# Optimization experiments

Hardware: AMD Instinct MI355X
Metric: run time of the kernel (lower is better)

Reference implementation:

```python
import jax, jax.numpy as jnp
import numpy as np

B, S, D = 2, 2048, 2048
H, KV, HD = 8, 1, 256          # num_heads, num_kv_heads, head_dim
ROPE_BASE = 10000.0
NEG_INF = -1e9


def _rope_cos_sin(position_ids, head_dim, base):
    # position_ids: [B, S] -> cos/sin: [B, S, head_dim]
    inv_freq = 1.0 / (base ** (jnp.arange(0, head_dim, 2, dtype=jnp.float32) / head_dim))
    freqs = position_ids.astype(jnp.float32)[..., None] * inv_freq  # [B,S,HD/2]
    emb = jnp.concatenate([freqs, freqs], axis=-1)                  # [B,S,HD]
    return jnp.cos(emb), jnp.sin(emb)


def _rotate_half(x):
    h = x.shape[-1] // 2
    return jnp.concatenate([-x[..., h:], x[..., :h]], axis=-1)


def _apply_rope(x, cos, sin):
    # x: [B,h,S,HD]; cos/sin: [B,S,HD]
    c = cos[:, None, :, :]
    s = sin[:, None, :, :]
    return x * c + _rotate_half(x) * s


def setup_inputs() -> dict:
    key = jax.random.key(0)
    ks = jax.random.split(key, 6)
    hidden_state = jax.random.normal(ks[0], (B, S, D), dtype=jnp.float32)
    # additive causal mask: 0 on/below diagonal, -inf above
    causal = jnp.tril(jnp.ones((S, S), dtype=bool))
    attention_mask = jnp.where(causal, 0.0, NEG_INF).astype(jnp.float32)[None, None]  # [B?1,1,S,S]
    attention_mask = jnp.broadcast_to(attention_mask, (B, 1, S, S))
    position_ids = jnp.broadcast_to(jnp.arange(S, dtype=jnp.int64)[None, :], (B, S))
    scale = 0.02
    Wq = jax.random.normal(ks[1], (D, H * HD), dtype=jnp.float32) * scale
    Wk = jax.random.normal(ks[2], (D, KV * HD), dtype=jnp.float32) * scale
    Wv = jax.random.normal(ks[3], (D, KV * HD), dtype=jnp.float32) * scale
    Wo = jax.random.normal(ks[4], (H * HD, D), dtype=jnp.float32) * scale
    return {"hidden_state": hidden_state, "attention_mask": attention_mask,
            "position_ids": position_ids, "Wq": Wq, "Wk": Wk, "Wv": Wv, "Wo": Wo}


def reference(hidden_state, attention_mask, position_ids, Wq, Wk, Wv, Wo):
    bsz, q_len, _ = hidden_state.shape
    n_rep = H // KV
    # projections
    q = (hidden_state @ Wq).reshape(bsz, q_len, H, HD).transpose(0, 2, 1, 3)   # [B,H,S,HD]
    k = (hidden_state @ Wk).reshape(bsz, q_len, KV, HD).transpose(0, 2, 1, 3)  # [B,KV,S,HD]
    v = (hidden_state @ Wv).reshape(bsz, q_len, KV, HD).transpose(0, 2, 1, 3)
    # RoPE
    cos, sin = _rope_cos_sin(position_ids, HD, ROPE_BASE)
    q = _apply_rope(q, cos, sin)
    k = _apply_rope(k, cos, sin)
    # GQA: repeat kv heads
    k = jnp.repeat(k, n_rep, axis=1)  # [B,H,S,HD]
    v = jnp.repeat(v, n_rep, axis=1)
    # eager attention with full score matrix (faithful to source)
    scores = jnp.einsum('bhqd,bhkd->bhqk', q, k) / jnp.sqrt(jnp.float32(HD))
    scores = scores + attention_mask
    attn = jax.nn.softmax(scores.astype(jnp.float32), axis=-1).astype(q.dtype)
    out = jnp.einsum('bhqk,bhkd->bhqd', attn, v)            # [B,H,S,HD]
    out = out.transpose(0, 2, 1, 3).reshape(bsz, q_len, H * HD)
    return out @ Wo
```

## Files before the change

### kernel.cpp

```cpp
#include <hip/hip_runtime.h>
#include <cstdint>
#include <cstddef>

#define B_   2
#define S_   2048
#define D_   2048
#define H_   8
#define HD_  256
#define M_   (B_ * S_)
#define NQ_  (H_ * HD_)
#define NKV_ 256

typedef unsigned short u16;
typedef __attribute__((ext_vector_type(8))) short short8v;
typedef __attribute__((ext_vector_type(4))) float f32x4;

__device__ __forceinline__ u16 f2bf_rn(float x) {
    unsigned int u = __float_as_uint(x);
    unsigned int r = u + 0x7FFFu + ((u >> 16) & 1u);
    return (u16)(r >> 16);
}
__device__ __forceinline__ float bf2f(u16 h) {
    return __uint_as_float(((unsigned int)h) << 16);
}

__device__ __forceinline__ void gll16(const u16* g, u16* l) {
    __builtin_amdgcn_global_load_lds(
        (const __attribute__((address_space(1))) void*)(g),
        (__attribute__((address_space(3))) void*)(l), 16, 0, 0);
}

__global__ __launch_bounds__(256) void split_kernel(const float* __restrict__ in,
                                                    u16* __restrict__ hi,
                                                    u16* __restrict__ lo)
{
    const size_t i = ((size_t)blockIdx.x * 256 + threadIdx.x) * 8;
    float4 v0 = *(const float4*)(in + i);
    float4 v1 = *(const float4*)(in + i + 4);
    float xs[8] = {v0.x, v0.y, v0.z, v0.w, v1.x, v1.y, v1.z, v1.w};
    unsigned int hv[4], lv[4];
#pragma unroll
    for (int k = 0; k < 4; ++k) {
        u16 h0 = f2bf_rn(xs[2 * k]);
        u16 h1 = f2bf_rn(xs[2 * k + 1]);
        u16 l0 = f2bf_rn(xs[2 * k] - bf2f(h0));
        u16 l1 = f2bf_rn(xs[2 * k + 1] - bf2f(h1));
        hv[k] = (unsigned int)h0 | ((unsigned int)h1 << 16);
        lv[k] = (unsigned int)l0 | ((unsigned int)l1 << 16);
    }
    *(uint4*)(hi + i) = make_uint4(hv[0], hv[1], hv[2], hv[3]);
    *(uint4*)(lo + i) = make_uint4(lv[0], lv[1], lv[2], lv[3]);
}

__global__ __launch_bounds__(256) void tsplit_kernel(const float* __restrict__ W,
                                                     u16* __restrict__ Th,
                                                     u16* __restrict__ Tl,
                                                     int K, int N)
{
    __shared__ float t[64][65];
    const int kt = blockIdx.x, nt = blockIdx.y;
    const int c4 = (threadIdx.x & 15) * 4;
    const int r  = threadIdx.x >> 4;

#pragma unroll
    for (int s = 0; s < 4; ++s) {
        const int kk = r + s * 16;
        float4 v = *(const float4*)(W + (size_t)(kt * 64 + kk) * N + nt * 64 + c4);
        t[kk][c4 + 0] = v.x;
        t[kk][c4 + 1] = v.y;
        t[kk][c4 + 2] = v.z;
        t[kk][c4 + 3] = v.w;
    }
    __syncthreads();
#pragma unroll
    for (int s = 0; s < 4; ++s) {
        const int nn = r + s * 16;
        unsigned int hv[2], lv[2];
#pragma unroll
        for (int p = 0; p < 2; ++p) {
            u16 h0, h1, l0, l1;
            float x0 = t[c4 + 2 * p][nn];
            float x1 = t[c4 + 2 * p + 1][nn];
            h0 = f2bf_rn(x0); l0 = f2bf_rn(x0 - bf2f(h0));
            h1 = f2bf_rn(x1); l1 = f2bf_rn(x1 - bf2f(h1));
            hv[p] = (unsigned int)h0 | ((unsigned int)h1 << 16);
            lv[p] = (unsigned int)l0 | ((unsigned int)l1 << 16);
        }
        u16* ph = Th + (size_t)(nt * 64 + nn) * K + kt * 64 + c4;
        u16* pl = Tl + (size_t)(nt * 64 + nn) * K + kt * 64 + c4;
        *(uint2*)ph = make_uint2(hv[0], hv[1]);
        *(uint2*)pl = make_uint2(lv[0], lv[1]);
    }
}

__device__ __forceinline__ void mfma_gemm_tile(
    const u16* __restrict__ Ah, const u16* __restrict__ Al,
    const u16* __restrict__ Bh, const u16* __restrict__ Bl,
    float* __restrict__ C, const int Kd, const int ldc,
    const int bm0, const int bn0)
{
    __shared__ u16 ldsAh[128 * 32];
    __shared__ u16 ldsAl[128 * 32];
    __shared__ u16 ldsBh[128 * 32];
    __shared__ u16 ldsBl[128 * 32];

    const int tid  = threadIdx.x;
    const int lane = tid & 63;
    const int w    = tid >> 6;
    const int wr   = w >> 1, wc = w & 1;

    const int srow = w * 32 + (lane >> 2);
    const int schk = (lane & 3) * 8;
    const u16* gAh = Ah + (size_t)(bm0 + srow) * Kd + schk;
    const u16* gAl = Al + (size_t)(bm0 + srow) * Kd + schk;
    const u16* gBh = Bh + (size_t)(bn0 + srow) * Kd + schk;
    const u16* gBl = Bl + (size_t)(bn0 + srow) * Kd + schk;

    f32x4 acc[4][4];
#pragma unroll
    for (int i = 0; i < 4; ++i)
#pragma unroll
        for (int j = 0; j < 4; ++j) acc[i][j] = (f32x4){0.f, 0.f, 0.f, 0.f};

    const int fr = lane & 15;
    const int kb = (lane >> 4) * 8;

    for (int k0 = 0; k0 < Kd; k0 += 32) {
        if (k0) __syncthreads();
#pragma unroll
        for (int c = 0; c < 2; ++c) {
            const size_t go = (size_t)(c * 16) * Kd + k0;
            const int lb = (w * 32 + c * 16) * 32;
            gll16(gAh + go, &ldsAh[lb]);
            gll16(gAl + go, &ldsAl[lb]);
            gll16(gBh + go, &ldsBh[lb]);
            gll16(gBl + go, &ldsBl[lb]);
        }
        __syncthreads();

        short8v a_h[4], a_l[4], b_h[4], b_l[4];
#pragma unroll
        for (int f = 0; f < 4; ++f) {
            const int ra = (wr * 64 + f * 16 + fr) * 32 + kb;
            const int rb = (wc * 64 + f * 16 + fr) * 32 + kb;
            a_h[f] = *(const short8v*)&ldsAh[ra];
            a_l[f] = *(const short8v*)&ldsAl[ra];
            b_h[f] = *(const short8v*)&ldsBh[rb];
            b_l[f] = *(const short8v*)&ldsBl[rb];
        }
#pragma unroll
        for (int i = 0; i < 4; ++i)
#pragma unroll
            for (int j = 0; j < 4; ++j) {
                acc[i][j] = __builtin_amdgcn_mfma_f32_16x16x32_bf16(a_h[i], b_h[j], acc[i][j], 0, 0, 0);
                acc[i][j] = __builtin_amdgcn_mfma_f32_16x16x32_bf16(a_h[i], b_l[j], acc[i][j], 0, 0, 0);
                acc[i][j] = __builtin_amdgcn_mfma_f32_16x16x32_bf16(a_l[i], b_h[j], acc[i][j], 0, 0, 0);
            }
    }

    const int cr = (lane >> 4) * 4;
    const int cc = lane & 15;
#pragma unroll
    for (int i = 0; i < 4; ++i)
#pragma unroll
        for (int j = 0; j < 4; ++j) {
#pragma unroll
            for (int r = 0; r < 4; ++r) {
                C[(size_t)(bm0 + wr * 64 + i * 16 + cr + r) * ldc
                  + (bn0 + wc * 64 + j * 16 + cc)] = acc[i][j][r];
            }
        }
}

__global__ __launch_bounds__(256, 2) void qkv_mfma_kernel(
    const u16* __restrict__ Xh, const u16* __restrict__ Xl,
    const u16* __restrict__ WqTh, const u16* __restrict__ WqTl,
    const u16* __restrict__ WkTh, const u16* __restrict__ WkTl,
    const u16* __restrict__ WvTh, const u16* __restrict__ WvTl,
    float* __restrict__ Qo, float* __restrict__ Ko, float* __restrict__ Vo)
{
    const int bn = blockIdx.x;
    const u16 *Bh, *Bl; float* C; int ldc, col0;
    if (bn < 16)      { Bh = WqTh; Bl = WqTl; C = Qo; ldc = NQ_;  col0 = bn * 128; }
    else if (bn < 18) { Bh = WkTh; Bl = WkTl; C = Ko; ldc = NKV_; col0 = (bn - 16) * 128; }
    else              { Bh = WvTh; Bl = WvTl; C = Vo; ldc = NKV_; col0 = (bn - 18) * 128; }
    mfma_gemm_tile(Xh, Xl, Bh, Bl, C, D_, ldc, blockIdx.y * 128, col0);
}

__global__ __launch_bounds__(256, 2) void out_mfma_kernel(
    const u16* __restrict__ Ch, const u16* __restrict__ Cl,
    const u16* __restrict__ WoTh, const u16* __restrict__ WoTl,
    float* __restrict__ Out)
{
    mfma_gemm_tile(Ch, Cl, WoTh, WoTl, Out, NQ_, D_, blockIdx.y * 128, blockIdx.x * 128);
}

__global__ __launch_bounds__(128) void rope_split_q_kernel(
    const float* __restrict__ Qw, u16* __restrict__ Qh, u16* __restrict__ Ql)
{
    const int row = blockIdx.x;
    const int d = threadIdx.x;
    const int s = row & (S_ - 1);

    const float expo = (float)(2 * d) / (float)HD_;
    const float inv_freq = 1.0f / powf(10000.0f, expo);
    float sn, c;
    sincosf((float)s * inv_freq, &sn, &c);

    const float* qr = Qw + (size_t)row * NQ_;
    u16* qhr = Qh + (size_t)row * NQ_;
    u16* qlr = Ql + (size_t)row * NQ_;
#pragma unroll
    for (int h = 0; h < H_; ++h) {
        float x0 = qr[h * HD_ + d];
        float x1 = qr[h * HD_ + d + 128];
        float y0 = x0 * c - x1 * sn;
        float y1 = x1 * c + x0 * sn;
        u16 h0 = f2bf_rn(y0), h1 = f2bf_rn(y1);
        qhr[h * HD_ + d]       = h0;
        qhr[h * HD_ + d + 128] = h1;
        qlr[h * HD_ + d]       = f2bf_rn(y0 - bf2f(h0));
        qlr[h * HD_ + d + 128] = f2bf_rn(y1 - bf2f(h1));
    }
}

__global__ __launch_bounds__(128) void rope_split_k_swz_kernel(
    const float* __restrict__ Kw, u16* __restrict__ Kh, u16* __restrict__ Kl,
    int* __restrict__ wq)
{
    if (blockIdx.x == 0 && threadIdx.x == 0) *wq = 0;

    const int row = blockIdx.x;
    const int d = threadIdx.x;
    const int s = row & (S_ - 1);
    const int xm = row & 7;

    const float expo = (float)(2 * d) / (float)HD_;
    const float inv_freq = 1.0f / powf(10000.0f, expo);
    float sn, c;
    sincosf((float)s * inv_freq, &sn, &c);

    const float* kr = Kw + (size_t)row * HD_;
    float x0 = kr[d], x1 = kr[d + 128];
    float y0 = x0 * c - x1 * sn;
    float y1 = x1 * c + x0 * sn;
    u16 h0 = f2bf_rn(y0), h1 = f2bf_rn(y1);

    const int o0 = (((d >> 3) ^ xm) << 3) | (d & 7);
    const int o1 = ((((d + 128) >> 3) ^ xm) << 3) | (d & 7);
    Kh[(size_t)row * HD_ + o0] = h0;
    Kh[(size_t)row * HD_ + o1] = h1;
    Kl[(size_t)row * HD_ + o0] = f2bf_rn(y0 - bf2f(h0));
    Kl[(size_t)row * HD_ + o1] = f2bf_rn(y1 - bf2f(h1));
}

#define KVB_ 32
#define PBS_ 44
#define NITEM_ 512

__global__ __launch_bounds__(256, 2) void attn_mfma_kernel(
    const u16* __restrict__ Qh, const u16* __restrict__ Ql,
    const u16* __restrict__ Kh, const u16* __restrict__ Kl,
    const u16* __restrict__ VtH, const u16* __restrict__ VtL,
    u16* __restrict__ Ch, u16* __restrict__ Cl,
    int* __restrict__ wq)
{
    __shared__ u16 kvK[2 * 32 * 256];
    __shared__ u16 kvV[2 * 256 * 32];
    __shared__ u16 pb[2 * 64 * PBS_];
    __shared__ int s_item;

    const int tid = threadIdx.x;
    const int lane = tid & 63;
    const int w = tid >> 6;

    const int fr = lane & 15;
    const int kq = (lane >> 4);
    const int xm = fr & 7;

    const int k_hi = (lane >> 5);
    const int k_ch = lane & 31;
    const int v_dl = w * 64 + (lane >> 2);
    const int v_cc = (lane & 3) * 8;

    while (true) {
        __syncthreads();
        if (tid == 0) s_item = atomicAdd(wq, 1);
        __syncthreads();
        const int item = s_item;
        if (item >= NITEM_) break;

        const int qt = 31 - (item >> 4);
        const int bh = item & 15;
        const int b = bh >> 3, h = bh & 7;

        short8v qfh[8], qfl[8];
        {
            const size_t qrow = (size_t)(b * S_ + qt * 64 + w * 16 + fr);
            const u16* ph = Qh + qrow * NQ_ + h * HD_ + kq * 8;
            const u16* pl = Ql + qrow * NQ_ + h * HD_ + kq * 8;
#pragma unroll
            for (int ks = 0; ks < 8; ++ks) {
                qfh[ks] = *(const short8v*)(ph + ks * 32);
                qfl[ks] = *(const short8v*)(pl + ks * 32);
            }
        }

        f32x4 oacc[16];
#pragma unroll
        for (int f = 0; f < 16; ++f) oacc[f] = (f32x4){0.f, 0.f, 0.f, 0.f};
        float m_i[4] = {-1e30f, -1e30f, -1e30f, -1e30f};
        float l_i[4] = {0.f, 0.f, 0.f, 0.f};

        const u16* ksrc[2] = {Kh + (size_t)b * S_ * HD_, Kl + (size_t)b * S_ * HD_};
        const u16* vsrc[2] = {VtH + (size_t)b * HD_ * S_, VtL + (size_t)b * HD_ * S_};

        const int nkt = (qt + 1) * 2;

#define STAGE_K(KT)                                                            \
        {                                                                      \
            _Pragma("unroll")                                                  \
            for (int c = 0; c < 2; ++c) {                                      \
                _Pragma("unroll")                                              \
                for (int t = 0; t < 4; ++t) {                                  \
                    const int rl = w * 8 + t * 2 + k_hi;                       \
                    gll16(ksrc[c] + (size_t)((KT) * KVB_ + rl) * HD_ + k_ch * 8, \
                          &kvK[c * 8192 + (w * 2048 + t * 512)]);              \
                }                                                              \
            }                                                                  \
        }

#define STAGE_V(KT)                                                            \
        {                                                                      \
            _Pragma("unroll")                                                  \
            for (int c = 0; c < 2; ++c) {                                      \
                _Pragma("unroll")                                              \
                for (int t = 0; t < 4; ++t) {                                  \
                    gll16(vsrc[c] + (size_t)(v_dl + t * 16) * S_ + (KT) * KVB_ + v_cc, \
                          &kvV[c * 8192 + (w * 2048 + t * 512)]);              \
                }                                                              \
            }                                                                  \
        }

        STAGE_K(0)
        STAGE_V(0)
        __syncthreads();

        for (int kt = 0; kt < nkt; ++kt) {
            const bool more = (kt + 1 < nkt);

            f32x4 s0 = (f32x4){0.f, 0.f, 0.f, 0.f};
            f32x4 s1 = (f32x4){0.f, 0.f, 0.f, 0.f};
#pragma unroll
            for (int ks = 0; ks < 8; ++ks) {
                const int ch = (ks * 4 + kq) ^ xm;
                short8v kh0 = *(const short8v*)&kvK[fr * 256 + ch * 8];
                short8v kh1 = *(const short8v*)&kvK[(16 + fr) * 256 + ch * 8];
                short8v kl0 = *(const short8v*)&kvK[8192 + fr * 256 + ch * 8];
                short8v kl1 = *(const short8v*)&kvK[8192 + (16 + fr) * 256 + ch * 8];
                s0 = __builtin_amdgcn_mfma_f32_16x16x32_bf16(qfh[ks], kh0, s0, 0, 0, 0);
                s1 = __builtin_amdgcn_mfma_f32_16x16x32_bf16(qfh[ks], kh1, s1, 0, 0, 0);
                s0 = __builtin_amdgcn_mfma_f32_16x16x32_bf16(qfh[ks], kl0, s0, 0, 0, 0);
                s1 = __builtin_amdgcn_mfma_f32_16x16x32_bf16(qfh[ks], kl1, s1, 0, 0, 0);
                s0 = __builtin_amdgcn_mfma_f32_16x16x32_bf16(qfl[ks], kh0, s0, 0, 0, 0);
                s1 = __builtin_amdgcn_mfma_f32_16x16x32_bf16(qfl[ks], kh1, s1, 0, 0, 0);
            }

            const int qglob = qt * 64 + w * 16 + kq * 4;
            const int kg = kt * KVB_ + fr;
            float x0v[4], x1v[4], mxl[4];
            bool needl = false;
#pragma unroll
            for (int r = 0; r < 4; ++r) {
                float x0 = s0[r] * 0.0625f;
                float x1 = s1[r] * 0.0625f;
                if (kg > qglob + r)      x0 = -1e30f;
                if (kg + 16 > qglob + r) x1 = -1e30f;
                x0v[r] = x0; x1v[r] = x1;
                mxl[r] = fmaxf(x0, x1);
                needl = needl || (mxl[r] > m_i[r] + 8.0f);
            }
            if (__any((int)needl)) {
#pragma unroll
                for (int r = 0; r < 4; ++r) {
                    float mx = mxl[r];
#pragma unroll
                    for (int off = 1; off < 16; off <<= 1)
                        mx = fmaxf(mx, __shfl_xor(mx, off, 64));
                    const float mnew = fmaxf(m_i[r], mx);
                    const float alpha = __expf(m_i[r] - mnew);
                    l_i[r] *= alpha;
                    m_i[r] = mnew;
#pragma unroll
                    for (int f = 0; f < 16; ++f) oacc[f][r] *= alpha;
                }
            }
#pragma unroll
            for (int r = 0; r < 4; ++r) {
                const float p0 = __expf(x0v[r] - m_i[r]);
                const float p1 = __expf(x1v[r] - m_i[r]);
                float ps = p0 + p1;
#pragma unroll
                for (int off = 1; off < 16; off <<= 1)
                    ps += __shfl_xor(ps, off, 64);
                l_i[r] += ps;

                const int prow = (w * 16 + kq * 4 + r) * PBS_;
                u16 h0 = f2bf_rn(p0), h1 = f2bf_rn(p1);
                pb[prow + fr]                    = h0;
                pb[prow + 16 + fr]               = h1;
                pb[64 * PBS_ + prow + fr]        = f2bf_rn(p0 - bf2f(h0));
                pb[64 * PBS_ + prow + 16 + fr]   = f2bf_rn(p1 - bf2f(h1));
            }
            __syncthreads();

            if (more) STAGE_K(kt + 1)

            {
                short8v pah = *(const short8v*)&pb[(w * 16 + fr) * PBS_ + kq * 8];
                short8v pal = *(const short8v*)&pb[64 * PBS_ + (w * 16 + fr) * PBS_ + kq * 8];
#pragma unroll
                for (int f = 0; f < 16; ++f) {
                    const int vrow = (f * 16 + fr) * 32 + kq * 8;
                    short8v vh = *(const short8v*)&kvV[vrow];
                    short8v vl = *(const short8v*)&kvV[8192 + vrow];
                    oacc[f] = __builtin_amdgcn_mfma_f32_16x16x32_bf16(pah, vh, oacc[f], 0, 0, 0);
                    oacc[f] = __builtin_amdgcn_mfma_f32_16x16x32_bf16(pal, vh, oacc[f], 0, 0, 0);
                    oacc[f] = __builtin_amdgcn_mfma_f32_16x16x32_bf16(pah, vl, oacc[f], 0, 0, 0);
                }
            }
            if (more) {
                __syncthreads();
                STAGE_V(kt + 1)
            }
        }

        {
            const size_t obase = (size_t)(b * S_ + qt * 64 + w * 16 + kq * 4) * NQ_ + h * HD_ + fr;
            u16* ohr = Ch + obase;
            u16* olr = Cl + obase;
#pragma unroll
            for (int r = 0; r < 4; ++r) {
                const float inv_l = 1.0f / l_i[r];
#pragma unroll
                for (int f = 0; f < 16; ++f) {
                    const float v = oacc[f][r] * inv_l;
                    const u16 hh = f2bf_rn(v);
                    ohr[(size_t)r * NQ_ + f * 16] = hh;
                    olr[(size_t)r * NQ_ + f * 16] = f2bf_rn(v - bf2f(hh));
                }
            }
        }
#undef STAGE_K
#undef STAGE_V
    }
}

extern "C" void kernel_launch(void* const* d_in, const int* in_sizes, int n_in,
                              void* d_out, int out_size, void* d_ws, size_t ws_size,
                              hipStream_t stream)
{
    (void)in_sizes; (void)n_in; (void)out_size; (void)ws_size;

    const float* hidden = (const float*)d_in[0];
    const float* Wq = (const float*)d_in[3];
    const float* Wk = (const float*)d_in[4];
    const float* Wv = (const float*)d_in[5];
    const float* Wo = (const float*)d_in[6];
    float* out = (float*)d_out;

    char* ws = (char*)d_ws;
    float* Qw = (float*)(ws + 0);
    u16* Kh2 = (u16*)(ws + 0);
    u16* Kl2 = (u16*)(ws + 2097152u);
    u16* VtH = (u16*)(ws + 4194304u);
    u16* VtL = (u16*)(ws + 6291456u);
    int* wq  = (int*)(ws + 8388608u);
    float* Kw = (float*)(ws + 33554432u);
    float* Vw = (float*)(ws + 37748736u);
    u16* Ch2 = (u16*)(ws + 41943040u);
    u16* Cl2 = (u16*)(ws + 58720256u);
    u16* Ah  = (u16*)(ws + 75497472u);
    u16* Al  = (u16*)(ws + 92274688u);
    u16* WqTh = (u16*)(ws + 109051904u);
    u16* WqTl = (u16*)(ws + 117440512u);
    u16* WkTh = (u16*)(ws + 125829120u);
    u16* WkTl = (u16*)(ws + 126877696u);
    u16* WvTh = (u16*)(ws + 127926272u);
    u16* WvTl = (u16*)(ws + 128974848u);
    u16* WoTh = WqTh;
    u16* WoTl = WqTl;
    u16* Qhb = Ah;
    u16* Qlb = Al;

    split_kernel<<<dim3((M_ * D_) / (256 * 8)), dim3(256), 0, stream>>>(hidden, Ah, Al);

    tsplit_kernel<<<dim3(D_ / 64, NQ_ / 64),  dim3(256), 0, stream>>>(Wq, WqTh, WqTl, D_, NQ_);
    tsplit_kernel<<<dim3(D_ / 64, NKV_ / 64), dim3(256), 0, stream>>>(Wk, WkTh, WkTl, D_, NKV_);
    tsplit_kernel<<<dim3(D_ / 64, NKV_ / 64), dim3(256), 0, stream>>>(Wv, WvTh, WvTl, D_, NKV_);

    qkv_mfma_kernel<<<dim3(20, M_ / 128), dim3(256), 0, stream>>>(
        Ah, Al, WqTh, WqTl, WkTh, WkTl, WvTh, WvTl, Qw, Kw, Vw);

    rope_split_q_kernel<<<dim3(M_), dim3(128), 0, stream>>>(Qw, Qhb, Qlb);
    rope_split_k_swz_kernel<<<dim3(M_), dim3(128), 0, stream>>>(Kw, Kh2, Kl2, wq);

    tsplit_kernel<<<dim3(S_ / 64, NKV_ / 64), dim3(256), 0, stream>>>(
        Vw, VtH, VtL, S_, NKV_);
    tsplit_kernel<<<dim3(S_ / 64, NKV_ / 64), dim3(256), 0, stream>>>(
        Vw + (size_t)S_ * NKV_, VtH + (size_t)HD_ * S_, VtL + (size_t)HD_ * S_, S_, NKV_);

    attn_mfma_kernel<<<dim3(256), dim3(256), 0, stream>>>(
        Qhb, Qlb, Kh2, Kl2, VtH, VtL, Ch2, Cl2, wq);

    tsplit_kernel<<<dim3(NQ_ / 64, D_ / 64), dim3(256), 0, stream>>>(Wo, WoTh, WoTl, NQ_, D_);

    out_mfma_kernel<<<dim3(D_ / 128, M_ / 128), dim3(256), 0, stream>>>(
        Ch2, Cl2, WoTh, WoTl, out);
}
```

Measured before the change: 579.2 us.

## Double-buffer K/V tiles in LDS and prefetch next tile at loop start

Doubles the K and V shared-memory buffers so the next KV tile is loaded asynchronously while the current one is used for QK^T and PV. This replaces the previous per-iteration pair of barriers with a single barrier at the end of each iteration. The mid-loop barrier can go because each wave writes and reads only its own rows of the P buffer. The larger LDS footprint likely drops residency to one block per CU, which is why the min-blocks launch bound is removed. That lost occupancy may cancel the gain from overlapping loads with compute.

```diff
diff --git a/kernel.cpp b/kernel.cpp
--- a/kernel.cpp
+++ b/kernel.cpp
@@ -258,15 +258,15 @@
 #define PBS_ 44
 #define NITEM_ 512
 
-__global__ __launch_bounds__(256, 2) void attn_mfma_kernel(
+__global__ __launch_bounds__(256) void attn_mfma_kernel(
     const u16* __restrict__ Qh, const u16* __restrict__ Ql,
     const u16* __restrict__ Kh, const u16* __restrict__ Kl,
     const u16* __restrict__ VtH, const u16* __restrict__ VtL,
     u16* __restrict__ Ch, u16* __restrict__ Cl,
     int* __restrict__ wq)
 {
-    __shared__ u16 kvK[2 * 32 * 256];
-    __shared__ u16 kvV[2 * 256 * 32];
+    __shared__ u16 kvK[2 * 2 * 32 * 256];
+    __shared__ u16 kvV[2 * 2 * 256 * 32];
     __shared__ u16 pb[2 * 64 * PBS_];
     __shared__ int s_item;
 
@@ -317,7 +317,7 @@
 
         const int nkt = (qt + 1) * 2;
 
-#define STAGE_K(KT)                                                            \
+#define STAGE_K(KT, BUF)                                                       \
         {                                                                      \
             _Pragma("unroll")                                                  \
             for (int c = 0; c < 2; ++c) {                                      \
@@ -325,39 +325,46 @@
                 for (int t = 0; t < 4; ++t) {                                  \
                     const int rl = w * 8 + t * 2 + k_hi;                       \
                     gll16(ksrc[c] + (size_t)((KT) * KVB_ + rl) * HD_ + k_ch * 8, \
-                          &kvK[c * 8192 + (w * 2048 + t * 512)]);              \
+                          &kvK[(BUF) * 16384 + c * 8192 + w * 2048 + t * 512]);  \
                 }                                                              \
             }                                                                  \
         }
 
-#define STAGE_V(KT)                                                            \
+#define STAGE_V(KT, BUF)                                                       \
         {                                                                      \
             _Pragma("unroll")                                                  \
             for (int c = 0; c < 2; ++c) {                                      \
                 _Pragma("unroll")                                              \
                 for (int t = 0; t < 4; ++t) {                                  \
                     gll16(vsrc[c] + (size_t)(v_dl + t * 16) * S_ + (KT) * KVB_ + v_cc, \
-                          &kvV[c * 8192 + (w * 2048 + t * 512)]);              \
+                          &kvV[(BUF) * 16384 + c * 8192 + w * 2048 + t * 512]);  \
                 }                                                              \
             }                                                                  \
         }
 
-        STAGE_K(0)
-        STAGE_V(0)
+        STAGE_K(0, 0)
+        STAGE_V(0, 0)
         __syncthreads();
 
+        int p = 0;
         for (int kt = 0; kt < nkt; ++kt) {
             const bool more = (kt + 1 < nkt);
 
+            if (more) {
+                STAGE_K(kt + 1, p ^ 1)
+                STAGE_V(kt + 1, p ^ 1)
+            }
+
+            const int kb0 = p * 16384;
             f32x4 s0 = (f32x4){0.f, 0.f, 0.f, 0.f};
             f32x4 s1 = (f32x4){0.f, 0.f, 0.f, 0.f};
 #pragma unroll
             for (int ks = 0; ks < 8; ++ks) {
                 const int ch = (ks * 4 + kq) ^ xm;
-                short8v kh0 = *(const short8v*)&kvK[fr * 256 + ch * 8];
-                short8v kh1 = *(const short8v*)&kvK[(16 + fr) * 256 + ch * 8];
-                short8v kl0 = *(const short8v*)&kvK[8192 + fr * 256 + ch * 8];
-                short8v kl1 = *(const short8v*)&kvK[8192 + (16 + fr) * 256 + ch * 8];
+                short8v kh0 = *(const short8v*)&kvK[kb0 + fr * 256 + ch * 8];
+                short8v kh1 = *(const short8v*)&kvK[kb0 + (16 + fr) * 256 + ch * 8];
+                short8v kl0 = *(const short8v*)&kvK[kb0 + 8192 + fr * 256 + ch * 8];
+                short8v kl1 = *(const short8v*)&kvK[kb0 + 8192 + (16 + fr) * 256 + ch * 8];
                 s0 = __builtin_amdgcn_mfma_f32_16x16x32_bf16(qfh[ks], kh0, s0, 0, 0, 0);
                 s1 = __builtin_amdgcn_mfma_f32_16x16x32_bf16(qfh[ks], kh1, s1, 0, 0, 0);
                 s0 = __builtin_amdgcn_mfma_f32_16x16x32_bf16(qfh[ks], kl0, s0, 0, 0, 0);
@@ -412,27 +419,24 @@
                 pb[64 * PBS_ + prow + fr]        = f2bf_rn(p0 - bf2f(h0));
                 pb[64 * PBS_ + prow + 16 + fr]   = f2bf_rn(p1 - bf2f(h1));
             }
-            __syncthreads();
-
-            if (more) STAGE_K(kt + 1)
 
             {
+                const int vb0 = p * 16384;
                 short8v pah = *(const short8v*)&pb[(w * 16 + fr) * PBS_ + kq * 8];
                 short8v pal = *(const short8v*)&pb[64 * PBS_ + (w * 16 + fr) * PBS_ + kq * 8];
 #pragma unroll
                 for (int f = 0; f < 16; ++f) {
-                    const int vrow = (f * 16 + fr) * 32 + kq * 8;
+                    const int vrow = vb0 + (f * 16 + fr) * 32 + kq * 8;
                     short8v vh = *(const short8v*)&kvV[vrow];
-                    short8v vl = *(const short8v*)&kvV[8192 + vrow];
+                    short8v vl = *(const short8v*)&kvV[vrow + 8192];
                     oacc[f] = __builtin_amdgcn_mfma_f32_16x16x32_bf16(pah, vh, oacc[f], 0, 0, 0);
                     oacc[f] = __builtin_amdgcn_mfma_f32_16x16x32_bf16(pal, vh, oacc[f], 0, 0, 0);
                     oacc[f] = __builtin_amdgcn_mfma_f32_16x16x32_bf16(pah, vl, oacc[f], 0, 0, 0);
                 }
             }
-            if (more) {
-                __syncthreads();
-                STAGE_V(kt + 1)
-            }
+
+            __syncthreads();
+            p ^= 1;
         }
 
         {
```

After: 587.9 us. Within noise of the previous version (+1.5%).
